# Kernel optimization log

Hardware: AMD Instinct MI355X
Metric: run time of the kernel (lower is better)

## Reference

```python
import jax, jax.numpy as jnp
import numpy as np

N_NODES = 50000
N_EDGES = 800000


def setup_inputs() -> dict:
    key = jax.random.key(0)
    ks = jax.random.split(key, 8)
    x = jax.random.normal(ks[0], (N_NODES, 128), dtype=jnp.float32)
    edge_index = jax.random.randint(ks[1], (2, N_EDGES), 0, N_NODES, dtype=jnp.int32)
    # Glorot-ish scaled weights
    W1 = jax.random.normal(ks[2], (128, 64), dtype=jnp.float32) / np.sqrt(128.0)
    b1 = jnp.zeros((64,), dtype=jnp.float32)
    W2 = jax.random.normal(ks[3], (64, 64), dtype=jnp.float32) / np.sqrt(64.0)
    b2 = jnp.zeros((64,), dtype=jnp.float32)
    W3 = jax.random.normal(ks[4], (64, 32), dtype=jnp.float32) / np.sqrt(64.0)
    b3 = jnp.zeros((32,), dtype=jnp.float32)
    return {"x": x, "edge_index": edge_index, "W1": W1, "b1": b1,
            "W2": W2, "b2": b2, "W3": W3, "b3": b3}


def _gcn_norm(edge_index, n_nodes):
    """Add self-loops and compute symmetric GCN edge normalization."""
    loop = jnp.arange(n_nodes, dtype=edge_index.dtype)
    src = jnp.concatenate([edge_index[0], loop])  # [E+N]
    dst = jnp.concatenate([edge_index[1], loop])
    deg = jax.ops.segment_sum(jnp.ones_like(dst, dtype=jnp.float32), dst,
                              num_segments=n_nodes)
    dis = jax.lax.rsqrt(jnp.maximum(deg, 1.0))  # deg >= 1 due to self-loops
    norm = dis[src] * dis[dst]                  # [E+N]
    return src, dst, norm


def _gcn_conv(h, W, b, src, dst, norm, n_nodes):
    # transform-then-aggregate (PyG GCNConv): messages have out_channels dim
    h = h @ W                                   # [N, out]
    msg = h[src] * norm[:, None]                # [E+N, out] gather + scale
    out = jax.ops.segment_sum(msg, dst, num_segments=n_nodes)  # scatter-add
    return out + b


def reference(x, edge_index, W1, b1, W2, b2, W3, b3):
    n = x.shape[0]
    src, dst, norm = _gcn_norm(edge_index, n)
    h = jax.nn.relu(_gcn_conv(x, W1, b1, src, dst, norm, n))
    # dropout is identity in eval mode
    h = jax.nn.relu(_gcn_conv(h, W2, b2, src, dst, norm, n))
    out = _gcn_conv(h, W3, b3, src, dst, norm, n)
    return out
```

## Files before the change

kernel.cpp:

```cpp
#include <hip/hip_runtime.h>
#include <hip/hip_fp16.h>


#define P3CAP 3200
#define P4CAP 8192

typedef float vf4 __attribute__((ext_vector_type(4)));

__device__ __forceinline__ int block_scan_incl(int v, int* s, int t) {
    s[t] = v;
    __syncthreads();
#pragma unroll
    for (int d = 1; d < 256; d <<= 1) {
        int a = (t >= d) ? s[t - d] : 0;
        __syncthreads();
        s[t] += a;
        __syncthreads();
    }
    return s[t];
}

__host__ __device__ __forceinline__ int chunk_of(int E) {
    return (((E + 255) / 256) + 3) & ~3;
}

__global__ __launch_bounds__(256) void part_hist_kernel(
    const int* __restrict__ dst, int* __restrict__ hist, int E, int nbuckets)
{
    __shared__ int lh[256];
    const int t = threadIdx.x;
    lh[t] = 0;
    __syncthreads();
    const int chunk = chunk_of(E);
    const int e0 = blockIdx.x * chunk;
    const int e1 = min(E, e0 + chunk);
    int e = e0 + t * 4;
    for (; e + 3 < e1; e += 1024) {
        const int4 d4 = *(const int4*)&dst[e];
        atomicAdd(&lh[d4.x >> 8], 1);
        atomicAdd(&lh[d4.y >> 8], 1);
        atomicAdd(&lh[d4.z >> 8], 1);
        atomicAdd(&lh[d4.w >> 8], 1);
    }
    for (; e < e1; ++e) atomicAdd(&lh[dst[e] >> 8], 1);
    __syncthreads();
    if (t < nbuckets) hist[t * 256 + blockIdx.x] = lh[t];
}

__global__ __launch_bounds__(256) void part_scan_kernel(
    const int* __restrict__ hist, int* __restrict__ hoff, int* __restrict__ btot)
{
    __shared__ int s[256];
    const int t = threadIdx.x;
    const int v = hist[blockIdx.x * 256 + t];
    const int inc = block_scan_incl(v, s, t);
    hoff[blockIdx.x * 256 + t] = inc - v;
    if (t == 255) btot[blockIdx.x] = inc;
}

__global__ __launch_bounds__(256) void part_scatter_kernel(
    const int* __restrict__ src, const int* __restrict__ dst,
    const int* __restrict__ hist, const int* __restrict__ hoff,
    const int* __restrict__ btot, int* __restrict__ bedge, int E, int nbuckets)
{
    __shared__ int gb[256], cur[256], s[256];
    __shared__ int stage[P3CAP];
    const int t = threadIdx.x;

    const int bv = (t < nbuckets) ? btot[t] : 0;
    const int binc = block_scan_incl(bv, s, t);
    const int bbase_t = binc - bv;
    __syncthreads();

    const int cnt_t = (t < nbuckets) ? hist[t * 256 + blockIdx.x] : 0;
    const int inc = block_scan_incl(cnt_t, s, t);
    const int excl = inc - cnt_t;
    cur[t] = excl;
    if (t < nbuckets) gb[t] = bbase_t + hoff[t * 256 + blockIdx.x] - excl;
    __syncthreads();

    const int chunk = chunk_of(E);
    const int e0 = blockIdx.x * chunk;
    const int e1 = min(E, e0 + chunk);
    {
        int e = e0 + t * 4;
        for (; e + 3 < e1; e += 1024) {
            const int4 d4 = *(const int4*)&dst[e];
            const int4 s4 = *(const int4*)&src[e];
            int r, b;
            b = d4.x >> 8; r = atomicAdd(&cur[b], 1);
            stage[r] = (s4.x & 0xffff) | ((d4.x & 255) << 16) | (b << 24);
            b = d4.y >> 8; r = atomicAdd(&cur[b], 1);
            stage[r] = (s4.y & 0xffff) | ((d4.y & 255) << 16) | (b << 24);
            b = d4.z >> 8; r = atomicAdd(&cur[b], 1);
            stage[r] = (s4.z & 0xffff) | ((d4.z & 255) << 16) | (b << 24);
            b = d4.w >> 8; r = atomicAdd(&cur[b], 1);
            stage[r] = (s4.w & 0xffff) | ((d4.w & 255) << 16) | (b << 24);
        }
        for (; e < e1; ++e) {
            const int dv = dst[e];
            const int b = dv >> 8;
            const int r = atomicAdd(&cur[b], 1);
            stage[r] = (src[e] & 0xffff) | ((dv & 255) << 16) | (b << 24);
        }
    }
    __syncthreads();
    const int cnt = e1 - e0;
    for (int i = t; i < cnt; i += 256) {
        const int p = stage[i];
        const int bucket = (int)((unsigned)p >> 24);
        bedge[gb[bucket] + i] = p;
    }
}

__global__ __launch_bounds__(256) void bucket_csr_kernel(
    const int* __restrict__ bedge, const int* __restrict__ btot,
    int* __restrict__ csr, int* __restrict__ off, float* __restrict__ dis,
    int N, int nbuckets)
{
    __shared__ int deg[256], cur[256], s[256];
    __shared__ int e01[2];
    __shared__ int ebuf[P4CAP];
    __shared__ int lcsr[P4CAP];
    const int t = threadIdx.x;
    const int b = blockIdx.x;

    const int bv = (t < nbuckets) ? btot[t] : 0;
    const int binc = block_scan_incl(bv, s, t);
    if (t == b) { e01[0] = binc - bv; e01[1] = binc; }
    deg[t] = 0;
    __syncthreads();
    const int e0 = e01[0], e1 = e01[1];
    const int m = e1 - e0;

    for (int i = t; i < m; i += 256) ebuf[i] = bedge[e0 + i];
    __syncthreads();
    for (int i = t; i < m; i += 256)
        atomicAdd(&deg[(ebuf[i] >> 16) & 255], 1);
    __syncthreads();
    const int v = deg[t];
    const int inc = block_scan_incl(v, s, t);
    cur[t] = inc - v;
    const int node = (b << 8) + t;
    if (node < N) {
        off[node + 1] = e0 + inc;
        dis[node] = rsqrtf((float)v + 1.0f);
        if (node == 0) off[0] = 0;
    }
    __syncthreads();
    for (int i = t; i < m; i += 256) {
        const int p = ebuf[i];
        const int pos = atomicAdd(&cur[(p >> 16) & 255], 1);
        lcsr[pos] = p & 0xffff;
    }
    __syncthreads();
    for (int i = t; i < m; i += 256)
        csr[e0 + i] = lcsr[i];
}

template<int K, int C, int TR>
__global__ __launch_bounds__(256) void gemm_scale_kernel(
    const float* __restrict__ in, const float* __restrict__ W,
    const float* __restrict__ dis, __half* __restrict__ hp, int N)
{
    constexpr int TX = C / 4;
    constexpr int R  = (256 / TX) * TR;
    __shared__ float Wl[K * C];

    const int t = threadIdx.x;
    for (int i = t; i < K * C / 4; i += 256)
        ((float4*)Wl)[i] = ((const float4*)W)[i];
    __syncthreads();

    const int tx = t % TX, ty = t / TX;
    const int cb = tx * 4;
    const int row0 = blockIdx.x * R + ty * TR;

    float acc[TR][4];
#pragma unroll
    for (int r = 0; r < TR; ++r) acc[r][0] = acc[r][1] = acc[r][2] = acc[r][3] = 0.0f;

    auto store_row = [&](int row, int r) {
        const float d = dis[row];
        __half2 h0 = __float22half2_rn(make_float2(acc[r][0] * d, acc[r][1] * d));
        __half2 h1 = __float22half2_rn(make_float2(acc[r][2] * d, acc[r][3] * d));
        uint2 u;
        u.x = *(unsigned*)&h0;
        u.y = *(unsigned*)&h1;
        *(uint2*)&hp[(size_t)row * C + cb] = u;
    };

    if (row0 + TR <= N) {
        const float* inp = in + (size_t)row0 * K;
#pragma unroll 4
        for (int k4 = 0; k4 < K / 4; ++k4) {
            float4 w0 = *(const float4*)&Wl[(k4 * 4 + 0) * C + cb];
            float4 w1 = *(const float4*)&Wl[(k4 * 4 + 1) * C + cb];
            float4 w2 = *(const float4*)&Wl[(k4 * 4 + 2) * C + cb];
            float4 w3 = *(const float4*)&Wl[(k4 * 4 + 3) * C + cb];
#pragma unroll
            for (int r = 0; r < TR; ++r) {
                const vf4 a = __builtin_nontemporal_load((const vf4*)&inp[r * K + k4 * 4]);
                acc[r][0] = fmaf(a.x, w0.x, acc[r][0]);
                acc[r][1] = fmaf(a.x, w0.y, acc[r][1]);
                acc[r][2] = fmaf(a.x, w0.z, acc[r][2]);
                acc[r][3] = fmaf(a.x, w0.w, acc[r][3]);
                acc[r][0] = fmaf(a.y, w1.x, acc[r][0]);
                acc[r][1] = fmaf(a.y, w1.y, acc[r][1]);
                acc[r][2] = fmaf(a.y, w1.z, acc[r][2]);
                acc[r][3] = fmaf(a.y, w1.w, acc[r][3]);
                acc[r][0] = fmaf(a.z, w2.x, acc[r][0]);
                acc[r][1] = fmaf(a.z, w2.y, acc[r][1]);
                acc[r][2] = fmaf(a.z, w2.z, acc[r][2]);
                acc[r][3] = fmaf(a.z, w2.w, acc[r][3]);
                acc[r][0] = fmaf(a.w, w3.x, acc[r][0]);
                acc[r][1] = fmaf(a.w, w3.y, acc[r][1]);
                acc[r][2] = fmaf(a.w, w3.z, acc[r][2]);
                acc[r][3] = fmaf(a.w, w3.w, acc[r][3]);
            }
        }
#pragma unroll
        for (int r = 0; r < TR; ++r) store_row(row0 + r, r);
    } else {
        for (int k = 0; k < K; ++k) {
            const float4 w4 = *(const float4*)&Wl[k * C + cb];
#pragma unroll
            for (int r = 0; r < TR; ++r) {
                const int row = row0 + r;
                const float a = (row < N) ? in[(size_t)row * K + k] : 0.0f;
                acc[r][0] = fmaf(a, w4.x, acc[r][0]);
                acc[r][1] = fmaf(a, w4.y, acc[r][1]);
                acc[r][2] = fmaf(a, w4.z, acc[r][2]);
                acc[r][3] = fmaf(a, w4.w, acc[r][3]);
            }
        }
#pragma unroll
        for (int r = 0; r < TR; ++r)
            if (row0 + r < N) store_row(row0 + r, r);
    }
}

template<int COUT>
__global__ __launch_bounds__(256) void fused_agg_gemm_kernel(
    const int* __restrict__ off, const int* __restrict__ csr,
    const float* __restrict__ dis, const __half* __restrict__ hp_in,
    const float* __restrict__ bias, const float* __restrict__ Wn,
    __half* __restrict__ hp_out, int N)
{
    constexpr int TX  = COUT / 4;
    constexpr int NPB = 256 / TX;
    constexpr int NPW = NPB / 4;
    __shared__ float Wl[64 * COUT];
    __shared__ float Al[NPB * 65];

    const int t = threadIdx.x;
    for (int i = t; i < 64 * COUT / 4; i += 256)
        ((float4*)Wl)[i] = ((const float4*)Wn)[i];

    const int wv   = t >> 6;
    const int lane = t & 63;
    const int grp  = lane >> 3;
    const int gl   = lane & 7;

    float b[8];
#pragma unroll
    for (int j = 0; j < 8; ++j) b[j] = bias[gl * 8 + j];

    auto accum = [](float4 v, float* a) {
        const __half2* h2 = (const __half2*)&v;
#pragma unroll
        for (int j = 0; j < 4; ++j) {
            const float2 pr = __half22float2(h2[j]);
            a[2 * j]     += pr.x;
            a[2 * j + 1] += pr.y;
        }
    };

    const int node0 = blockIdx.x * NPB + wv * NPW;
    for (int nl = 0; nl < NPW; ++nl) {
        const int node = node0 + nl;
        if (node >= N) break;
        const int s0 = off[node];
        const int s1 = off[node + 1];

        float acc[8]  = {0, 0, 0, 0, 0, 0, 0, 0};
        float acc2[8] = {0, 0, 0, 0, 0, 0, 0, 0};

        if (grp == 0) {
            const float4 v = *(const float4*)&hp_in[(size_t)node * 64 + gl * 8];
            accum(v, acc);
        }
        int e = s0 + grp;
        for (; e + 8 < s1; e += 16) {
            const int sa = csr[e];
            const int sb = csr[e + 8];
            const float4 va = *(const float4*)&hp_in[(size_t)sa * 64 + gl * 8];
            const float4 vb = *(const float4*)&hp_in[(size_t)sb * 64 + gl * 8];
            accum(va, acc);
            accum(vb, acc2);
        }
        if (e < s1) {
            const int sa = csr[e];
            const float4 va = *(const float4*)&hp_in[(size_t)sa * 64 + gl * 8];
            accum(va, acc);
        }
#pragma unroll
        for (int j = 0; j < 8; ++j) acc[j] += acc2[j];
#pragma unroll
        for (int d = 8; d < 64; d <<= 1) {
#pragma unroll
            for (int j = 0; j < 8; ++j) acc[j] += __shfl_xor(acc[j], d);
        }
        if (grp == 0) {
            const float dn = dis[node];
            const int row = wv * NPW + nl;
#pragma unroll
            for (int j = 0; j < 8; ++j)
                Al[row * 65 + gl * 8 + j] = fmaxf(fmaf(dn, acc[j], b[j]), 0.0f);
        }
    }
    __syncthreads();

    const int tx = t % TX, ty = t / TX;
    const int gnode = blockIdx.x * NPB + ty;
    const int cb = tx * 4;
    float c0 = 0.f, c1 = 0.f, c2 = 0.f, c3 = 0.f;
#pragma unroll 8
    for (int k = 0; k < 64; ++k) {
        const float a = Al[ty * 65 + k];
        const float4 w4 = *(const float4*)&Wl[k * COUT + cb];
        c0 = fmaf(a, w4.x, c0);
        c1 = fmaf(a, w4.y, c1);
        c2 = fmaf(a, w4.z, c2);
        c3 = fmaf(a, w4.w, c3);
    }
    if (gnode < N) {
        const float d = dis[gnode];
        __half2 h0 = __float22half2_rn(make_float2(c0 * d, c1 * d));
        __half2 h1 = __float22half2_rn(make_float2(c2 * d, c3 * d));
        uint2 u;
        u.x = *(unsigned*)&h0;
        u.y = *(unsigned*)&h1;
        *(uint2*)&hp_out[(size_t)gnode * COUT + cb] = u;
    }
}

template<int C, bool RELU>
__global__ __launch_bounds__(256) void agg_kernel(
    const int* __restrict__ off, const int* __restrict__ csr,
    const float* __restrict__ dis, const __half* __restrict__ hp,
    const float* __restrict__ bias, float* __restrict__ out, int N)
{
    constexpr int GL = C / 8;
    constexpr int G  = 64 / GL;
    const int wv   = threadIdx.x >> 6;
    const int lane = threadIdx.x & 63;
    const int grp  = lane / GL;
    const int gl   = lane % GL;
    const int node = blockIdx.x * 4 + wv;
    if (node >= N) return;

    const int s0 = off[node];
    const int s1 = off[node + 1];

    float acc[8]  = {0, 0, 0, 0, 0, 0, 0, 0};
    float acc2[8] = {0, 0, 0, 0, 0, 0, 0, 0};

    auto accum = [](float4 v, float* a) {
        const __half2* h2 = (const __half2*)&v;
#pragma unroll
        for (int j = 0; j < 4; ++j) {
            const float2 pr = __half22float2(h2[j]);
            a[2 * j]     += pr.x;
            a[2 * j + 1] += pr.y;
        }
    };

    if (grp == 0) {
        const float4 v = *(const float4*)&hp[(size_t)node * C + gl * 8];
        accum(v, acc);
    }
    int e = s0 + grp;
    for (; e + G < s1; e += 2 * G) {
        const int sa = csr[e];
        const int sb = csr[e + G];
        const float4 va = *(const float4*)&hp[(size_t)sa * C + gl * 8];
        const float4 vb = *(const float4*)&hp[(size_t)sb * C + gl * 8];
        accum(va, acc);
        accum(vb, acc2);
    }
    if (e < s1) {
        const int sa = csr[e];
        const float4 va = *(const float4*)&hp[(size_t)sa * C + gl * 8];
        accum(va, acc);
    }
#pragma unroll
    for (int j = 0; j < 8; ++j) acc[j] += acc2[j];

#pragma unroll
    for (int d = GL; d < 64; d <<= 1) {
#pragma unroll
        for (int j = 0; j < 8; ++j) acc[j] += __shfl_xor(acc[j], d);
    }

    if (grp == 0) {
        const float dn = dis[node];
        float v[8];
#pragma unroll
        for (int j = 0; j < 8; ++j) {
            v[j] = fmaf(dn, acc[j], bias[gl * 8 + j]);
            if (RELU) v[j] = fmaxf(v[j], 0.f);
        }
        *(float4*)&out[(size_t)node * C + gl * 8]     = make_float4(v[0], v[1], v[2], v[3]);
        *(float4*)&out[(size_t)node * C + gl * 8 + 4] = make_float4(v[4], v[5], v[6], v[7]);
    }
}

static inline size_t align_up(size_t x) { return (x + 255) & ~(size_t)255; }

extern "C" void kernel_launch(void* const* d_in, const int* in_sizes, int n_in,
                              void* d_out, int out_size, void* d_ws, size_t ws_size,
                              hipStream_t stream) {
    const float* x   = (const float*)d_in[0];
    const int*  eidx = (const int*)d_in[1];
    const float* W1  = (const float*)d_in[2];
    const float* b1  = (const float*)d_in[3];
    const float* W2  = (const float*)d_in[4];
    const float* b2  = (const float*)d_in[5];
    const float* W3  = (const float*)d_in[6];
    const float* b3  = (const float*)d_in[7];
    float* out = (float*)d_out;

    const int N = in_sizes[0] / 128;
    const int E = in_sizes[1] / 2;
    const int* srcp = eidx;
    const int* dstp = eidx + E;
    const int nbuckets = (N + 255) >> 8;

    char* ws = (char*)d_ws;
    size_t o = 0;
    float* dis   = (float*)(ws + o);  o = align_up(o + (size_t)N * 4);
    int* off     = (int*)(ws + o);    o = align_up(o + (size_t)(N + 1) * 4);
    int* btot    = (int*)(ws + o);    o = align_up(o + 256 * 4);
    int* hist    = (int*)(ws + o);    o = align_up(o + 256 * 256 * 4);
    int* hoff    = (int*)(ws + o);    o = align_up(o + 256 * 256 * 4);
    int* bedge   = (int*)(ws + o);    o = align_up(o + (size_t)E * 4);
    int* csr     = (int*)(ws + o);    o = align_up(o + (size_t)E * 4);
    __half* H1   = (__half*)(ws + o); o = align_up(o + (size_t)N * 64 * 2);
    __half* H2   = (__half*)(ws + o); o = align_up(o + (size_t)N * 64 * 2);
    __half* H3   = H1;

    const dim3 blk(256);

    part_hist_kernel<<<dim3(256), blk, 0, stream>>>(dstp, hist, E, nbuckets);
    part_scan_kernel<<<dim3(nbuckets), blk, 0, stream>>>(hist, hoff, btot);
    part_scatter_kernel<<<dim3(256), blk, 0, stream>>>(srcp, dstp, hist, hoff, btot, bedge, E, nbuckets);
    bucket_csr_kernel<<<dim3(nbuckets), blk, 0, stream>>>(bedge, btot, csr, off, dis, N, nbuckets);

    gemm_scale_kernel<128, 64, 2><<<dim3((N + 31) / 32), blk, 0, stream>>>(x, W1, dis, H1, N);

    fused_agg_gemm_kernel<64><<<dim3((N + 15) / 16), blk, 0, stream>>>(
        off, csr, dis, H1, b1, W2, H2, N);
    fused_agg_gemm_kernel<32><<<dim3((N + 31) / 32), blk, 0, stream>>>(
        off, csr, dis, H2, b2, W3, H3, N);
    agg_kernel<32, false><<<dim3((N + 3) / 4), blk, 0, stream>>>(off, csr, dis, H3, b3, out, N);
}
```

Measured before the change: 213.2 us.

## Fuse partition histogram, scan and scatter using atomic bucket reservation; shrink CSR indices

Replaces the three-kernel partition step (histogram, per-bucket scan, scatter) with one kernel. Each block counts its edges per bucket locally and reserves space in a fixed-capacity per-bucket slab with a global atomicAdd. This removes two launches and the hist/hoff round trips, but edge order within a bucket now depends on block timing and a bucket is capped at BCAP entries. CSR indices are also stored as 16-bit values to halve index traffic in the aggregation kernels, which relies on node ids fitting in 16 bits.

Measured after the change: 213.7 us. No clear change (+0.3%).

```diff
diff --git a/kernel.cpp b/kernel.cpp
--- a/kernel.cpp
+++ b/kernel.cpp
@@ -4,6 +4,7 @@
 
 #define P3CAP 3200
 #define P4CAP 8192
+#define BCAP  8192
 
 typedef float vf4 __attribute__((ext_vector_type(4)));
 
@@ -24,64 +25,36 @@
     return (((E + 255) / 256) + 3) & ~3;
 }
 
-__global__ __launch_bounds__(256) void part_hist_kernel(
-    const int* __restrict__ dst, int* __restrict__ hist, int E, int nbuckets)
+__global__ __launch_bounds__(256) void part_sort_reserve_kernel(
+    const int* __restrict__ src, const int* __restrict__ dst,
+    int* __restrict__ btot, int* __restrict__ bedge, int E, int nbuckets)
 {
-    __shared__ int lh[256];
+    __shared__ int lh[256], gb[256], cur[256], s[256];
+    __shared__ int stage[P3CAP];
     const int t = threadIdx.x;
+
     lh[t] = 0;
     __syncthreads();
     const int chunk = chunk_of(E);
     const int e0 = blockIdx.x * chunk;
     const int e1 = min(E, e0 + chunk);
-    int e = e0 + t * 4;
-    for (; e + 3 < e1; e += 1024) {
-        const int4 d4 = *(const int4*)&dst[e];
-        atomicAdd(&lh[d4.x >> 8], 1);
-        atomicAdd(&lh[d4.y >> 8], 1);
-        atomicAdd(&lh[d4.z >> 8], 1);
-        atomicAdd(&lh[d4.w >> 8], 1);
-    }
-    for (; e < e1; ++e) atomicAdd(&lh[dst[e] >> 8], 1);
-    __syncthreads();
-    if (t < nbuckets) hist[t * 256 + blockIdx.x] = lh[t];
-}
-
-__global__ __launch_bounds__(256) void part_scan_kernel(
-    const int* __restrict__ hist, int* __restrict__ hoff, int* __restrict__ btot)
-{
-    __shared__ int s[256];
-    const int t = threadIdx.x;
-    const int v = hist[blockIdx.x * 256 + t];
-    const int inc = block_scan_incl(v, s, t);
-    hoff[blockIdx.x * 256 + t] = inc - v;
-    if (t == 255) btot[blockIdx.x] = inc;
-}
-
-__global__ __launch_bounds__(256) void part_scatter_kernel(
-    const int* __restrict__ src, const int* __restrict__ dst,
-    const int* __restrict__ hist, const int* __restrict__ hoff,
-    const int* __restrict__ btot, int* __restrict__ bedge, int E, int nbuckets)
-{
-    __shared__ int gb[256], cur[256], s[256];
-    __shared__ int stage[P3CAP];
-    const int t = threadIdx.x;
-
-    const int bv = (t < nbuckets) ? btot[t] : 0;
-    const int binc = block_scan_incl(bv, s, t);
-    const int bbase_t = binc - bv;
-    __syncthreads();
-
-    const int cnt_t = (t < nbuckets) ? hist[t * 256 + blockIdx.x] : 0;
+    {
+        int e = e0 + t * 4;
+        for (; e + 3 < e1; e += 1024) {
+            const int4 d4 = *(const int4*)&dst[e];
+            atomicAdd(&lh[d4.x >> 8], 1);
+            atomicAdd(&lh[d4.y >> 8], 1);
+            atomicAdd(&lh[d4.z >> 8], 1);
+            atomicAdd(&lh[d4.w >> 8], 1);
+        }
+        for (; e < e1; ++e) atomicAdd(&lh[dst[e] >> 8], 1);
+    }
+    __syncthreads();
+    const int cnt_t = lh[t];
     const int inc = block_scan_incl(cnt_t, s, t);
     const int excl = inc - cnt_t;
     cur[t] = excl;
-    if (t < nbuckets) gb[t] = bbase_t + hoff[t * 256 + blockIdx.x] - excl;
-    __syncthreads();
-
-    const int chunk = chunk_of(E);
-    const int e0 = blockIdx.x * chunk;
-    const int e1 = min(E, e0 + chunk);
+    __syncthreads();
     {
         int e = e0 + t * 4;
         for (; e + 3 < e1; e += 1024) {
@@ -104,6 +77,11 @@
             stage[r] = (src[e] & 0xffff) | ((dv & 255) << 16) | (b << 24);
         }
     }
+    if (t < nbuckets) {
+        int base = 0;
+        if (cnt_t > 0) base = atomicAdd(&btot[t], cnt_t);
+        gb[t] = t * BCAP + base - excl;
+    }
     __syncthreads();
     const int cnt = e1 - e0;
     for (int i = t; i < cnt; i += 256) {
@@ -115,13 +93,13 @@
 
 __global__ __launch_bounds__(256) void bucket_csr_kernel(
     const int* __restrict__ bedge, const int* __restrict__ btot,
-    int* __restrict__ csr, int* __restrict__ off, float* __restrict__ dis,
-    int N, int nbuckets)
+    unsigned short* __restrict__ csr, int* __restrict__ off,
+    float* __restrict__ dis, int N, int nbuckets)
 {
     __shared__ int deg[256], cur[256], s[256];
     __shared__ int e01[2];
     __shared__ int ebuf[P4CAP];
-    __shared__ int lcsr[P4CAP];
+    __shared__ unsigned short lcsr[P4CAP];
     const int t = threadIdx.x;
     const int b = blockIdx.x;
 
@@ -133,7 +111,7 @@
     const int e0 = e01[0], e1 = e01[1];
     const int m = e1 - e0;
 
-    for (int i = t; i < m; i += 256) ebuf[i] = bedge[e0 + i];
+    for (int i = t; i < m; i += 256) ebuf[i] = bedge[b * BCAP + i];
     __syncthreads();
     for (int i = t; i < m; i += 256)
         atomicAdd(&deg[(ebuf[i] >> 16) & 255], 1);
@@ -151,7 +129,7 @@
     for (int i = t; i < m; i += 256) {
         const int p = ebuf[i];
         const int pos = atomicAdd(&cur[(p >> 16) & 255], 1);
-        lcsr[pos] = p & 0xffff;
+        lcsr[pos] = (unsigned short)(p & 0xffff);
     }
     __syncthreads();
     for (int i = t; i < m; i += 256)
@@ -242,7 +220,7 @@
 
 template<int COUT>
 __global__ __launch_bounds__(256) void fused_agg_gemm_kernel(
-    const int* __restrict__ off, const int* __restrict__ csr,
+    const int* __restrict__ off, const unsigned short* __restrict__ csr,
     const float* __restrict__ dis, const __half* __restrict__ hp_in,
     const float* __restrict__ bias, const float* __restrict__ Wn,
     __half* __restrict__ hp_out, int N)
@@ -347,7 +325,7 @@
 
 template<int C, bool RELU>
 __global__ __launch_bounds__(256) void agg_kernel(
-    const int* __restrict__ off, const int* __restrict__ csr,
+    const int* __restrict__ off, const unsigned short* __restrict__ csr,
     const float* __restrict__ dis, const __half* __restrict__ hp,
     const float* __restrict__ bias, float* __restrict__ out, int N)
 {
@@ -439,22 +417,19 @@
 
     char* ws = (char*)d_ws;
     size_t o = 0;
-    float* dis   = (float*)(ws + o);  o = align_up(o + (size_t)N * 4);
-    int* off     = (int*)(ws + o);    o = align_up(o + (size_t)(N + 1) * 4);
-    int* btot    = (int*)(ws + o);    o = align_up(o + 256 * 4);
-    int* hist    = (int*)(ws + o);    o = align_up(o + 256 * 256 * 4);
-    int* hoff    = (int*)(ws + o);    o = align_up(o + 256 * 256 * 4);
-    int* bedge   = (int*)(ws + o);    o = align_up(o + (size_t)E * 4);
-    int* csr     = (int*)(ws + o);    o = align_up(o + (size_t)E * 4);
-    __half* H1   = (__half*)(ws + o); o = align_up(o + (size_t)N * 64 * 2);
-    __half* H2   = (__half*)(ws + o); o = align_up(o + (size_t)N * 64 * 2);
-    __half* H3   = H1;
+    float* dis          = (float*)(ws + o);          o = align_up(o + (size_t)N * 4);
+    int* off            = (int*)(ws + o);            o = align_up(o + (size_t)(N + 1) * 4);
+    int* btot           = (int*)(ws + o);            o = align_up(o + 256 * 4);
+    int* bedge          = (int*)(ws + o);            o = align_up(o + (size_t)nbuckets * BCAP * 4);
+    unsigned short* csr = (unsigned short*)(ws + o); o = align_up(o + (size_t)E * 2);
+    __half* H1          = (__half*)(ws + o);         o = align_up(o + (size_t)N * 64 * 2);
+    __half* H2          = (__half*)(ws + o);         o = align_up(o + (size_t)N * 64 * 2);
+    __half* H3          = H1;
 
     const dim3 blk(256);
 
-    part_hist_kernel<<<dim3(256), blk, 0, stream>>>(dstp, hist, E, nbuckets);
-    part_scan_kernel<<<dim3(nbuckets), blk, 0, stream>>>(hist, hoff, btot);
-    part_scatter_kernel<<<dim3(256), blk, 0, stream>>>(srcp, dstp, hist, hoff, btot, bedge, E, nbuckets);
+    hipMemsetAsync(btot, 0, 256 * sizeof(int), stream);
+    part_sort_reserve_kernel<<<dim3(256), blk, 0, stream>>>(srcp, dstp, btot, bedge, E, nbuckets);
     bucket_csr_kernel<<<dim3(nbuckets), blk, 0, stream>>>(bedge, btot, csr, off, dis, N, nbuckets);
 
     gemm_scale_kernel<128, 64, 2><<<dim3((N + 31) / 32), blk, 0, stream>>>(x, W1, dis, H1, N);
```
